# Kernel tuning notes

Measured on AMD Instinct MI355X. Metric: run time of the kernel, lower is better.

The kernel has to match this reference:

```python
import jax, jax.numpy as jnp
import numpy as np


def setup_inputs() -> dict:
    key = jax.random.key(0)
    k1, k2 = jax.random.split(key)
    N, D, G = 2_000_000, 128, 1024
    node_h = jax.random.normal(k1, (N, D), dtype=jnp.float32)
    node_batch = jnp.sort(jax.random.randint(k2, (N,), 0, G, dtype=jnp.int64))
    return {"node_h": node_h, "node_batch": node_batch, "num_graphs": G}


def reference(node_h, node_batch, num_graphs):
    # scatter(node_h, node_batch, dim=0, dim_size=num_graphs, reduce='mean')
    sums = jax.ops.segment_sum(node_h, node_batch, num_segments=num_graphs)
    counts = jax.ops.segment_sum(
        jnp.ones((node_h.shape[0],), dtype=node_h.dtype),
        node_batch, num_segments=num_graphs)
    # empty segments yield 0 (torch_scatter mean divides by clamped count)
    graph_h = sums / jnp.maximum(counts, 1.0)[:, None]
    return graph_h
```

## Files before the change

kernel.cpp:

```cpp
#include <hip/hip_runtime.h>


__global__ __launch_bounds__(256) void seg_mean_kernel(
    const float* __restrict__ h,
    const int* __restrict__ batch,
    float* __restrict__ out,
    int N) {
  const int g = blockIdx.x;

  int lo = 0, hi = N;
  while (lo < hi) {
    int mid = (lo + hi) >> 1;
    if (batch[mid] < g) lo = mid + 1; else hi = mid;
  }
  const int start = lo;
  hi = N;
  while (lo < hi) {
    int mid = (lo + hi) >> 1;
    if (batch[mid] < g + 1) lo = mid + 1; else hi = mid;
  }
  const int end = lo;
  const int rows = end - start;

  const int tid = threadIdx.x;
  const int c = tid & 31;
  const int r = tid >> 5;

  float4 acc = make_float4(0.f, 0.f, 0.f, 0.f);
  const float* base = h + (size_t)start * 128 + (size_t)c * 4;

  int i = r;
  for (; i + 8 < rows; i += 16) {
    const float4 v0 = *(const float4*)(base + (size_t)i * 128);
    const float4 v1 = *(const float4*)(base + (size_t)(i + 8) * 128);
    acc.x += v0.x; acc.y += v0.y; acc.z += v0.z; acc.w += v0.w;
    acc.x += v1.x; acc.y += v1.y; acc.z += v1.z; acc.w += v1.w;
  }
  if (i < rows) {
    const float4 v = *(const float4*)(base + (size_t)i * 128);
    acc.x += v.x; acc.y += v.y; acc.z += v.z; acc.w += v.w;
  }

  __shared__ float4 smem[256];
  smem[tid] = acc;
  __syncthreads();

  if (r == 0) {
    float4 s = smem[c];
    #pragma unroll
    for (int k = 1; k < 8; ++k) {
      const float4 v = smem[k * 32 + c];
      s.x += v.x; s.y += v.y; s.z += v.z; s.w += v.w;
    }
    const float inv = 1.0f / (float)(rows > 0 ? rows : 1);
    float4 o;
    o.x = s.x * inv; o.y = s.y * inv; o.z = s.z * inv; o.w = s.w * inv;
    *(float4*)(out + (size_t)g * 128 + (size_t)c * 4) = o;
  }
}

extern "C" void kernel_launch(void* const* d_in, const int* in_sizes, int n_in,
                              void* d_out, int out_size, void* d_ws, size_t ws_size,
                              hipStream_t stream) {
  const float* node_h   = (const float*)d_in[0];
  const int*   batch    = (const int*)d_in[1];
  float*       out      = (float*)d_out;

  const int N = in_sizes[1];
  const int D = in_sizes[0] / N;
  const int G = out_size / D;

  seg_mean_kernel<<<G, 256, 0, stream>>>(node_h, batch, out, N);
}
```

Before: 1.271 ms.

## Split each segment across eight blocks with precomputed offsets and two-stage reduction

Moves the segment boundary binary searches into a separate kernel that writes an offsets array once. It then launches eight blocks per graph, each summing an interleaved share of the segment's rows with 4-way unrolled loads into a workspace of partials. A final kernel combines the partials and divides by the count. This raises parallelism from 1024 blocks to 8192 so the memory-bound reduction can better saturate bandwidth, at the cost of two extra launches and a small partials round-trip.

```diff
diff --git a/kernel.cpp b/kernel.cpp
--- a/kernel.cpp
+++ b/kernel.cpp
@@ -1,43 +1,51 @@
 #include <hip/hip_runtime.h>
 
 
-__global__ __launch_bounds__(256) void seg_mean_kernel(
-    const float* __restrict__ h,
-    const int* __restrict__ batch,
-    float* __restrict__ out,
-    int N) {
-  const int g = blockIdx.x;
+#define SPLIT 8
 
+__global__ __launch_bounds__(256) void seg_offsets_kernel(
+    const int* __restrict__ batch, int* __restrict__ offs, int N, int G) {
+  const int g = blockIdx.x * 256 + threadIdx.x;
+  if (g > G) return;
   int lo = 0, hi = N;
   while (lo < hi) {
-    int mid = (lo + hi) >> 1;
+    const int mid = (lo + hi) >> 1;
     if (batch[mid] < g) lo = mid + 1; else hi = mid;
   }
-  const int start = lo;
-  hi = N;
-  while (lo < hi) {
-    int mid = (lo + hi) >> 1;
-    if (batch[mid] < g + 1) lo = mid + 1; else hi = mid;
-  }
-  const int end = lo;
-  const int rows = end - start;
+  offs[g] = lo;
+}
 
-  const int tid = threadIdx.x;
-  const int c = tid & 31;
-  const int r = tid >> 5;
+__global__ __launch_bounds__(256) void seg_partial_kernel(
+    const float* __restrict__ h,
+    const int* __restrict__ offs,
+    float* __restrict__ partials) {
+  const int g = blockIdx.x >> 3;
+  const int s = blockIdx.x & 7;
+  const int start = offs[g];
+  const int end   = offs[g + 1];
+
+  const int tid  = threadIdx.x;
+  const int c    = tid & 31;
+  const int r    = tid >> 5;
+  const int slot = s * 8 + r;
 
   float4 acc = make_float4(0.f, 0.f, 0.f, 0.f);
-  const float* base = h + (size_t)start * 128 + (size_t)c * 4;
 
-  int i = r;
-  for (; i + 8 < rows; i += 16) {
-    const float4 v0 = *(const float4*)(base + (size_t)i * 128);
-    const float4 v1 = *(const float4*)(base + (size_t)(i + 8) * 128);
-    acc.x += v0.x; acc.y += v0.y; acc.z += v0.z; acc.w += v0.w;
-    acc.x += v1.x; acc.y += v1.y; acc.z += v1.z; acc.w += v1.w;
+  int row = start + slot;
+  const float* p = h + (size_t)row * 128 + (size_t)c * 4;
+
+  for (; row + 192 < end; row += 256, p += 32768) {
+    const float4 v0 = *(const float4*)(p);
+    const float4 v1 = *(const float4*)(p + 8192);
+    const float4 v2 = *(const float4*)(p + 16384);
+    const float4 v3 = *(const float4*)(p + 24576);
+    acc.x += v0.x + v1.x + v2.x + v3.x;
+    acc.y += v0.y + v1.y + v2.y + v3.y;
+    acc.z += v0.z + v1.z + v2.z + v3.z;
+    acc.w += v0.w + v1.w + v2.w + v3.w;
   }
-  if (i < rows) {
-    const float4 v = *(const float4*)(base + (size_t)i * 128);
+  for (; row < end; row += 64, p += 8192) {
+    const float4 v = *(const float4*)(p);
     acc.x += v.x; acc.y += v.y; acc.z += v.z; acc.w += v.w;
   }
 
@@ -46,15 +54,42 @@
   __syncthreads();
 
   if (r == 0) {
-    float4 s = smem[c];
+    float4 sum = smem[c];
     #pragma unroll
     for (int k = 1; k < 8; ++k) {
       const float4 v = smem[k * 32 + c];
-      s.x += v.x; s.y += v.y; s.z += v.z; s.w += v.w;
+      sum.x += v.x; sum.y += v.y; sum.z += v.z; sum.w += v.w;
     }
-    const float inv = 1.0f / (float)(rows > 0 ? rows : 1);
+    *(float4*)(partials + (size_t)blockIdx.x * 128 + (size_t)c * 4) = sum;
+  }
+}
+
+__global__ __launch_bounds__(256) void seg_final_kernel(
+    const float* __restrict__ partials,
+    const int* __restrict__ offs,
+    float* __restrict__ out) {
+  const int g   = blockIdx.x;
+  const int tid = threadIdx.x;
+  const int c   = tid & 31;
+  const int r   = tid >> 5;
+
+  const float4 v =
+      *(const float4*)(partials + ((size_t)g * 8 + r) * 128 + (size_t)c * 4);
+  __shared__ float4 smem[256];
+  smem[tid] = v;
+  __syncthreads();
+
+  if (r == 0) {
+    float4 sum = smem[c];
+    #pragma unroll
+    for (int k = 1; k < 8; ++k) {
+      const float4 w = smem[k * 32 + c];
+      sum.x += w.x; sum.y += w.y; sum.z += w.z; sum.w += w.w;
+    }
+    const int cnt = offs[g + 1] - offs[g];
+    const float inv = 1.0f / (float)(cnt > 0 ? cnt : 1);
     float4 o;
-    o.x = s.x * inv; o.y = s.y * inv; o.z = s.z * inv; o.w = s.w * inv;
+    o.x = sum.x * inv; o.y = sum.y * inv; o.z = sum.z * inv; o.w = sum.w * inv;
     *(float4*)(out + (size_t)g * 128 + (size_t)c * 4) = o;
   }
 }
@@ -62,13 +97,18 @@
 extern "C" void kernel_launch(void* const* d_in, const int* in_sizes, int n_in,
                               void* d_out, int out_size, void* d_ws, size_t ws_size,
                               hipStream_t stream) {
-  const float* node_h   = (const float*)d_in[0];
-  const int*   batch    = (const int*)d_in[1];
-  float*       out      = (float*)d_out;
+  const float* node_h = (const float*)d_in[0];
+  const int*   batch  = (const int*)d_in[1];
+  float*       out    = (float*)d_out;
 
   const int N = in_sizes[1];
   const int D = in_sizes[0] / N;
   const int G = out_size / D;
 
-  seg_mean_kernel<<<G, 256, 0, stream>>>(node_h, batch, out, N);
+  int*   offs     = (int*)d_ws;
+  float* partials = (float*)((char*)d_ws + 8192);
+
+  seg_offsets_kernel<<<(G + 1 + 255) / 256, 256, 0, stream>>>(batch, offs, N, G);
+  seg_partial_kernel<<<G * SPLIT, 256, 0, stream>>>(node_h, offs, partials);
+  seg_final_kernel<<<G, 256, 0, stream>>>(partials, offs, out);
 }
```

New measurement: 1.262 ms. About the same (-0.7%).
